# Kernel tuning notes

Measured on AMD Instinct MI355X. Metric: run time of the kernel, lower is better.

## Reference

```python
import jax, jax.numpy as jnp
import numpy as np

DIM = 512
HEAD_DIM = 32
NUM_HEADS = DIM // HEAD_DIM
SCALE = HEAD_DIM ** -0.5
SPARSE_WINDOW = 64
LN_EPS = 1e-5


def setup_inputs() -> dict:
    key = jax.random.key(0)
    ks = jax.random.split(key, 7)
    B, S = 2, 2048
    x = jax.random.normal(ks[0], (B, S, DIM), dtype=jnp.float32)
    # parameters (Linear weights stored as [in, out] for x @ W)
    W_qkv = jax.random.normal(ks[1], (DIM, 2 * DIM), dtype=jnp.float32) * (DIM ** -0.5)
    b_qkv = jnp.zeros((2 * DIM,), dtype=jnp.float32)
    W_out = jax.random.normal(ks[2], (DIM, DIM), dtype=jnp.float32) * (DIM ** -0.5)
    b_out = jnp.zeros((DIM,), dtype=jnp.float32)
    ln_gamma = jnp.ones((DIM,), dtype=jnp.float32)
    ln_beta = jnp.zeros((DIM,), dtype=jnp.float32)
    return {"x": x, "W_qkv": W_qkv, "b_qkv": b_qkv, "W_out": W_out,
            "b_out": b_out, "ln_gamma": ln_gamma, "ln_beta": ln_beta}


def _attn(x, W_qkv, b_qkv, W_out, b_out, ln_gamma, ln_beta):
    B, S, _ = x.shape
    qkv = x @ W_qkv + b_qkv                        # [B,S,2*DIM]
    qk, v = qkv[..., :DIM], qkv[..., DIM:]
    q = jax.nn.silu(qk) * SCALE                    # shared-projection nonlinear Q
    k = jnp.tanh(qk)                               # shared-projection nonlinear K
    q = q.reshape(B, S, NUM_HEADS, HEAD_DIM)
    k = k.reshape(B, S, NUM_HEADS, HEAD_DIM)
    v = v.reshape(B, S, NUM_HEADS, HEAD_DIM)
    scores = jnp.einsum('bihd,bjhd->bhij', q, k)   # [B,H,S,S]
    # sparse window: MULTIPLICATIVE zeroing outside |i-j|<=w (faithful to source)
    i = jnp.arange(S)
    band = (jnp.abs(i[:, None] - i[None, :]) <= SPARSE_WINDOW).astype(scores.dtype)
    scores = scores * band                         # zeros still enter softmax as exp(0)
    probs = jax.nn.softmax(scores, axis=-1)
    out = jnp.einsum('bhij,bjhd->bihd', probs, v).reshape(B, S, DIM)
    out = out @ W_out + b_out
    y = x + out                                    # residual (dropout is eval no-op)
    mu = jnp.mean(y, axis=-1, keepdims=True)
    var = jnp.var(y, axis=-1, keepdims=True)
    return (y - mu) * jax.lax.rsqrt(var + LN_EPS) * ln_gamma + ln_beta


def reference(x, W_qkv, b_qkv, W_out, b_out, ln_gamma, ln_beta):
    return _attn(x, W_qkv, b_qkv, W_out, b_out, ln_gamma, ln_beta)
```

## Files before the change

kernel.cpp:

```cpp
#include <hip/hip_runtime.h>
#include <cstdint>
#include <cstddef>

#define DIMX 512
#define HDIM 32
#define NHEADS 16
#define SEQ 2048
#define BATCH 2
#define MTOT (BATCH*SEQ)
#define WIN 64
#define QSCALE 0.17677669529663687f

typedef __bf16 bf16x8 __attribute__((ext_vector_type(8)));
typedef float f32x4 __attribute__((ext_vector_type(4)));

__device__ __forceinline__ unsigned short f2bf(float f){
  unsigned u = __builtin_bit_cast(unsigned, f);
  u += 0x7FFFu + ((u >> 16) & 1u);
  return (unsigned short)(u >> 16);
}
__device__ __forceinline__ float bf2f(unsigned short s){
  return __builtin_bit_cast(float, ((unsigned)s) << 16);
}
__device__ __forceinline__ unsigned pk(float a, float b){
  return (unsigned)f2bf(a) | ((unsigned)f2bf(b) << 16);
}

__device__ __forceinline__ void gl_lds16(const void* g, void* l){
  __builtin_amdgcn_global_load_lds(
      (const __attribute__((address_space(1))) unsigned*)g,
      (__attribute__((address_space(3))) unsigned*)(unsigned)(unsigned long long)l,
      16, 0, 0);
}

__global__ void k_prep(const float* __restrict__ x, unsigned short* __restrict__ xb,
                       const float* __restrict__ Wq, unsigned short* __restrict__ Wqt,
                       const float* __restrict__ Wo, unsigned short* __restrict__ Wot){
  int bx = blockIdx.x;
  if (bx < 1024){
    int i = bx * 256 + threadIdx.x;
    const float4* p = (const float4*)x + (size_t)i * 2;
    float4 a = p[0], b = p[1];
    uint4 o;
    o.x = pk(a.x, a.y); o.y = pk(a.z, a.w);
    o.z = pk(b.x, b.y); o.w = pk(b.z, b.w);
    ((uint4*)xb)[i] = o;
    return;
  }
  __shared__ float tile[32][33];
  int i = bx - 1024;
  int bxx = i % 48, byy = i / 48;
  const float* W; unsigned short* Wt; int N, n0;
  if (bxx < 32){ W = Wq; Wt = Wqt; N = 1024; n0 = bxx * 32; }
  else         { W = Wo; Wt = Wot; N = 512;  n0 = (bxx - 32) * 32; }
  int k0 = byy * 32;
  int tx = threadIdx.x & 31, ty = threadIdx.x >> 5;
  #pragma unroll
  for (int r = 0; r < 32; r += 8)
    tile[ty + r][tx] = W[(size_t)(k0 + ty + r) * N + n0 + tx];
  __syncthreads();
  #pragma unroll
  for (int r = 0; r < 32; r += 8)
    Wt[(size_t)(n0 + ty + r) * 512 + k0 + tx] = f2bf(tile[tx][ty + r]);
}

template<int MODE, int NBN>
__launch_bounds__(256)
__global__ void k_gemm(const unsigned short* __restrict__ A,
                       const unsigned short* __restrict__ Bt,
                       const float* __restrict__ bias,
                       unsigned short* __restrict__ qb,
                       unsigned short* __restrict__ kb,
                       unsigned short* __restrict__ vt,
                       float* __restrict__ vsum_p,
                       const float* __restrict__ xres,
                       float* __restrict__ y)
{
  const int K = 512;
  constexpr int NWG = 64 * NBN;
  __shared__ __align__(16) unsigned short lds[2][2][64 * 64];
  int tid = threadIdx.x;
  int wid = tid >> 6, lane = tid & 63;
  int wm = wid >> 1, wn = wid & 1;
  int lane15 = lane & 15, laneh = lane >> 4;

  int g = blockIdx.x;
  int gwi = (g & 7) * (NWG / 8) + (g >> 3);
  int bm = gwi / NBN, bn = gwi % NBN;

  f32x4 acc[2][2] = {};

  int srow_off = lane >> 3;
  int spos     = lane & 7;

  auto STAGE = [&](int buf, int kt){
    int k0 = kt * 64;
    #pragma unroll
    for (int c = 0; c < 2; ++c){
      int cidx = wid * 2 + c;
      int r = cidx * 8 + srow_off;
      int ch = spos ^ (r & 7);
      gl_lds16(A  + (size_t)(bm * 64 + r) * K + k0 + ch * 8, &lds[buf][0][cidx * 512]);
      gl_lds16(Bt + (size_t)(bn * 64 + r) * K + k0 + ch * 8, &lds[buf][1][cidx * 512]);
    }
  };

  auto COMPUTE = [&](int buf){
    #pragma unroll
    for (int kh = 0; kh < 2; ++kh){
      int chunk = kh * 4 + laneh;
      bf16x8 af[2], bf[2];
      #pragma unroll
      for (int mi = 0; mi < 2; ++mi){
        int row = wm * 32 + mi * 16 + lane15;
        af[mi] = *(const bf16x8*)&lds[buf][0][row * 64 + (chunk ^ (row & 7)) * 8];
      }
      #pragma unroll
      for (int ni = 0; ni < 2; ++ni){
        int row = wn * 32 + ni * 16 + lane15;
        bf[ni] = *(const bf16x8*)&lds[buf][1][row * 64 + (chunk ^ (row & 7)) * 8];
      }
      #pragma unroll
      for (int mi = 0; mi < 2; ++mi)
        #pragma unroll
        for (int ni = 0; ni < 2; ++ni)
          acc[mi][ni] = __builtin_amdgcn_mfma_f32_16x16x32_bf16(af[mi], bf[ni], acc[mi][ni], 0, 0, 0);
    }
  };

  STAGE(0, 0);
  __syncthreads();
  #pragma unroll
  for (int kt = 0; kt < 8; ++kt){
    if (kt < 7) STAGE((kt + 1) & 1, kt + 1);
    COMPUTE(kt & 1);
    __syncthreads();
  }

  if (MODE == 0 && bn >= 8){
    unsigned short (*tp)[72] = (unsigned short (*)[72])&lds[0][0][0];
    #pragma unroll
    for (int mi = 0; mi < 2; ++mi)
      #pragma unroll
      for (int ni = 0; ni < 2; ++ni)
        #pragma unroll
        for (int r = 0; r < 4; ++r){
          int ml = wm * 32 + mi * 16 + laneh * 4 + r;
          int nl = wn * 32 + ni * 16 + lane15;
          tp[nl][ml] = f2bf(acc[mi][ni][r] + bias[bn * 64 + nl]);
        }
    __syncthreads();
    int nl = tid >> 2, q = tid & 3;
    int h = (bn - 8) * 2 + (nl >> 5), d = nl & 31;
    int bh = (bm >> 5) * 16 + h;
    int sc = bm & 31;
    unsigned short vals[16];
    float ssum = 0.f;
    #pragma unroll
    for (int j = 0; j < 16; ++j){ vals[j] = tp[nl][q * 16 + j]; ssum += bf2f(vals[j]); }
    ssum += __shfl_xor(ssum, 1); ssum += __shfl_xor(ssum, 2);
    uint4 o0, o1;
    o0.x = (unsigned)vals[0]  | ((unsigned)vals[1]  << 16);
    o0.y = (unsigned)vals[2]  | ((unsigned)vals[3]  << 16);
    o0.z = (unsigned)vals[4]  | ((unsigned)vals[5]  << 16);
    o0.w = (unsigned)vals[6]  | ((unsigned)vals[7]  << 16);
    o1.x = (unsigned)vals[8]  | ((unsigned)vals[9]  << 16);
    o1.y = (unsigned)vals[10] | ((unsigned)vals[11] << 16);
    o1.z = (unsigned)vals[12] | ((unsigned)vals[13] << 16);
    o1.w = (unsigned)vals[14] | ((unsigned)vals[15] << 16);
    size_t vtoff = (size_t)(bh * HDIM + d) * SEQ + sc * 64 + q * 16;
    *(uint4*)(vt + vtoff) = o0;
    *(uint4*)(vt + vtoff + 8) = o1;
    if (q == 0) vsum_p[(sc * 32 + bh) * HDIM + d] = ssum;
  } else {
    #pragma unroll
    for (int mi = 0; mi < 2; ++mi){
      #pragma unroll
      for (int ni = 0; ni < 2; ++ni){
        #pragma unroll
        for (int r = 0; r < 4; ++r){
          int m = bm * 64 + wm * 32 + mi * 16 + laneh * 4 + r;
          int n = bn * 64 + wn * 32 + ni * 16 + lane15;
          float val = acc[mi][ni][r] + bias[n];
          if (MODE == 0){
            float s = val / (1.0f + __expf(-val)) * QSCALE;
            float t = tanhf(val);
            qb[(size_t)m * DIMX + n] = f2bf(s);
            kb[(size_t)m * DIMX + n] = f2bf(t);
          } else {
            size_t idx = (size_t)m * DIMX + n;
            y[idx] = val + xres[idx];
          }
        }
      }
    }
  }
}

__launch_bounds__(256)
__global__ void k_attn(const unsigned short* __restrict__ qb,
                       const unsigned short* __restrict__ kb,
                       const unsigned short* __restrict__ vt,
                       const float* __restrict__ vsum_p,
                       unsigned short* __restrict__ ao)
{
  __shared__ unsigned short p_lds[4][16][40];
  int tid = threadIdx.x, wid = tid >> 6, lane = tid & 63;
  int lane15 = lane & 15, laneh = lane >> 4;
  int bh = blockIdx.y, b = bh >> 4, h = bh & 15;
  int s0 = blockIdx.x * 64 + wid * 16;

  bf16x8 qf = *(const bf16x8*)(qb + (size_t)(b * SEQ + s0 + lane15) * DIMX + h * HDIM + laneh * 8);
  float vs0 = 0.f, vs1 = 0.f;
  #pragma unroll
  for (int c = 0; c < 32; ++c){
    vs0 += vsum_p[(c * 32 + bh) * HDIM + lane15];
    vs1 += vsum_p[(c * 32 + bh) * HDIM + 16 + lane15];
  }

  f32x4 accv[2] = {};
  float dsum[4] = {0.f, 0.f, 0.f, 0.f};

  for (int jt = 0; jt < 9; ++jt){
    int j0 = s0 - 64 + jt * 16;
    int jc = min(max(j0 + lane15, 0), SEQ - 1);
    bf16x8 kf = *(const bf16x8*)(kb + (size_t)(b * SEQ + jc) * DIMX + h * HDIM + laneh * 8);
    f32x4 z = {0.f, 0.f, 0.f, 0.f};
    f32x4 sv = __builtin_amdgcn_mfma_f32_16x16x32_bf16(qf, kf, z, 0, 0, 0);
    #pragma unroll
    for (int r = 0; r < 4; ++r){
      int i = s0 + laneh * 4 + r;
      int j = j0 + lane15;
      int dj = i - j;
      bool inb = (dj <= WIN) && (dj >= -WIN) && (j >= 0) && (j < SEQ);
      float w = inb ? (__expf(sv[r]) - 1.0f) : 0.0f;
      dsum[r] += w;
      p_lds[wid][laneh * 4 + r][(jt & 1) * 16 + lane15] = f2bf(w);
    }
    if (jt & 1){
      int jc0 = j0 - 16;
      bf16x8 pa = *(const bf16x8*)&p_lds[wid][lane15][laneh * 8];
      int jv = min(max(jc0 + laneh * 8, 0), SEQ - 8);
      bf16x8 v0 = *(const bf16x8*)(vt + (size_t)(bh * HDIM + lane15) * SEQ + jv);
      bf16x8 v1 = *(const bf16x8*)(vt + (size_t)(bh * HDIM + 16 + lane15) * SEQ + jv);
      accv[0] = __builtin_amdgcn_mfma_f32_16x16x32_bf16(pa, v0, accv[0], 0, 0, 0);
      accv[1] = __builtin_amdgcn_mfma_f32_16x16x32_bf16(pa, v1, accv[1], 0, 0, 0);
    }
  }
  {
    #pragma unroll
    for (int r = 0; r < 4; ++r)
      p_lds[wid][laneh * 4 + r][16 + lane15] = 0;
    int jc0 = s0 + 64;
    bf16x8 pa = *(const bf16x8*)&p_lds[wid][lane15][laneh * 8];
    int jv = min(max(jc0 + laneh * 8, 0), SEQ - 8);
    bf16x8 v0 = *(const bf16x8*)(vt + (size_t)(bh * HDIM + lane15) * SEQ + jv);
    bf16x8 v1 = *(const bf16x8*)(vt + (size_t)(bh * HDIM + 16 + lane15) * SEQ + jv);
    accv[0] = __builtin_amdgcn_mfma_f32_16x16x32_bf16(pa, v0, accv[0], 0, 0, 0);
    accv[1] = __builtin_amdgcn_mfma_f32_16x16x32_bf16(pa, v1, accv[1], 0, 0, 0);
  }

  #pragma unroll
  for (int r = 0; r < 4; ++r){
    float v = dsum[r];
    v += __shfl_xor(v, 1); v += __shfl_xor(v, 2);
    v += __shfl_xor(v, 4); v += __shfl_xor(v, 8);
    dsum[r] = v;
  }
  #pragma unroll
  for (int r = 0; r < 4; ++r){
    int i = s0 + laneh * 4 + r;
    float dn = (float)SEQ + dsum[r];
    float o0 = (accv[0][r] + vs0) / dn;
    float o1 = (accv[1][r] + vs1) / dn;
    size_t base = (size_t)(b * SEQ + i) * DIMX + h * HDIM;
    ao[base + lane15]      = f2bf(o0);
    ao[base + 16 + lane15] = f2bf(o1);
  }
}

__global__ void k_ln(const float* __restrict__ y, const float* __restrict__ gamma,
                     const float* __restrict__ beta, float* __restrict__ out){
  int wid = threadIdx.x >> 6, lane = threadIdx.x & 63;
  int row = blockIdx.x * 4 + wid;
  const float4* yp = (const float4*)(y + (size_t)row * DIMX);
  float4 a = yp[lane], c = yp[lane + 64];
  float s  = a.x + a.y + a.z + a.w + c.x + c.y + c.z + c.w;
  float ss = a.x*a.x + a.y*a.y + a.z*a.z + a.w*a.w + c.x*c.x + c.y*c.y + c.z*c.z + c.w*c.w;
  #pragma unroll
  for (int m = 1; m < 64; m <<= 1){ s += __shfl_xor(s, m); ss += __shfl_xor(ss, m); }
  float mu = s * (1.f / DIMX);
  float var = ss * (1.f / DIMX) - mu * mu;
  float inv = rsqrtf(var + 1e-5f);
  const float4* gp = (const float4*)gamma;
  const float4* bp = (const float4*)beta;
  float4 g0 = gp[lane], g1 = gp[lane + 64];
  float4 b0 = bp[lane], b1 = bp[lane + 64];
  float4 o0, o1;
  o0.x = (a.x - mu) * inv * g0.x + b0.x; o0.y = (a.y - mu) * inv * g0.y + b0.y;
  o0.z = (a.z - mu) * inv * g0.z + b0.z; o0.w = (a.w - mu) * inv * g0.w + b0.w;
  o1.x = (c.x - mu) * inv * g1.x + b1.x; o1.y = (c.y - mu) * inv * g1.y + b1.y;
  o1.z = (c.z - mu) * inv * g1.z + b1.z; o1.w = (c.w - mu) * inv * g1.w + b1.w;
  float4* op = (float4*)(out + (size_t)row * DIMX);
  op[lane] = o0; op[lane + 64] = o1;
}

extern "C" void kernel_launch(void* const* d_in, const int* in_sizes, int n_in,
                              void* d_out, int out_size, void* d_ws, size_t ws_size,
                              hipStream_t stream){
  const float* x      = (const float*)d_in[0];
  const float* W_qkv  = (const float*)d_in[1];
  const float* b_qkv  = (const float*)d_in[2];
  const float* W_out  = (const float*)d_in[3];
  const float* b_out  = (const float*)d_in[4];
  const float* gamma  = (const float*)d_in[5];
  const float* beta   = (const float*)d_in[6];
  float* out = (float*)d_out;

  char* ws = (char*)d_ws;
  size_t off = 0;
  auto alloc = [&](size_t bytes){ void* p = ws + off; off += (bytes + 255) & ~(size_t)255; return p; };
  unsigned short* xb  = (unsigned short*)alloc((size_t)MTOT * DIMX * 2);
  unsigned short* wqt = (unsigned short*)alloc((size_t)1024 * 512 * 2);
  unsigned short* wot = (unsigned short*)alloc((size_t)512 * 512 * 2);
  unsigned short* qb  = (unsigned short*)alloc((size_t)MTOT * DIMX * 2);
  unsigned short* kb  = (unsigned short*)alloc((size_t)MTOT * DIMX * 2);
  unsigned short* vt  = (unsigned short*)alloc((size_t)32 * HDIM * SEQ * 2);
  float*          vsm = (float*)alloc((size_t)32 * 32 * HDIM * 4);
  unsigned short* ao  = (unsigned short*)alloc((size_t)MTOT * DIMX * 2);
  float*          yb  = (float*)alloc((size_t)MTOT * DIMX * 4);

  k_prep<<<1792, 256, 0, stream>>>(x, xb, W_qkv, wqt, W_out, wot);
  k_gemm<0, 16><<<1024, 256, 0, stream>>>(xb, wqt, b_qkv, qb, kb, vt, vsm, nullptr, nullptr);
  k_attn<<<dim3(32, 32), 256, 0, stream>>>(qb, kb, vt, vsm, ao);
  k_gemm<1, 8><<<512, 256, 0, stream>>>(ao, wot, b_out, nullptr, nullptr, nullptr, nullptr, x, yb);
  k_ln  <<<MTOT / 4, 256, 0, stream>>>(yb, gamma, beta, out);
}
```

Baseline: 51.59 us.

## Enlarge QKV GEMM M-tile to 128 and store residual intermediate in bf16

The GEMM is templated on the M-tile size. The QKV projection now uses 128-row tiles in 512 workgroups, which halves the partial V-sum chunks and widens the V transpose stores to 32 elements per thread. The output projection now reads the bf16 copy of x as its residual and writes y in bf16, so the LayerNorm kernel reads half the bytes. Both changes aim to cut memory traffic and launch granularity, at the cost of fewer workgroups for the QKV GEMM and extra rounding of the residual and pre-LayerNorm values to bf16.

```diff
diff --git a/kernel.cpp b/kernel.cpp
--- a/kernel.cpp
+++ b/kernel.cpp
@@ -64,7 +64,7 @@
     Wt[(size_t)(n0 + ty + r) * 512 + k0 + tx] = f2bf(tile[tx][ty + r]);
 }
 
-template<int MODE, int NBN>
+template<int MODE, int BM, int NBM, int NBN>
 __launch_bounds__(256)
 __global__ void k_gemm(const unsigned short* __restrict__ A,
                        const unsigned short* __restrict__ Bt,
@@ -73,12 +73,14 @@
                        unsigned short* __restrict__ kb,
                        unsigned short* __restrict__ vt,
                        float* __restrict__ vsum_p,
-                       const float* __restrict__ xres,
-                       float* __restrict__ y)
+                       const unsigned short* __restrict__ xb,
+                       unsigned short* __restrict__ yb)
 {
   const int K = 512;
-  constexpr int NWG = 64 * NBN;
-  __shared__ __align__(16) unsigned short lds[2][2][64 * 64];
+  constexpr int NWG = NBM * NBN;
+  constexpr int MF  = BM / 32;
+  __shared__ __align__(16) unsigned short ldsA[2][BM * 64];
+  __shared__ __align__(16) unsigned short ldsB[2][64 * 64];
   int tid = threadIdx.x;
   int wid = tid >> 6, lane = tid & 63;
   int wm = wid >> 1, wn = wid & 1;
@@ -88,20 +90,26 @@
   int gwi = (g & 7) * (NWG / 8) + (g >> 3);
   int bm = gwi / NBN, bn = gwi % NBN;
 
-  f32x4 acc[2][2] = {};
+  f32x4 acc[MF][2] = {};
 
   int srow_off = lane >> 3;
   int spos     = lane & 7;
 
   auto STAGE = [&](int buf, int kt){
     int k0 = kt * 64;
+    #pragma unroll
+    for (int c = 0; c < MF; ++c){
+      int cidx = wid * MF + c;
+      int r = cidx * 8 + srow_off;
+      int ch = spos ^ (r & 7);
+      gl_lds16(A + (size_t)(bm * BM + r) * K + k0 + ch * 8, &ldsA[buf][cidx * 512]);
+    }
     #pragma unroll
     for (int c = 0; c < 2; ++c){
       int cidx = wid * 2 + c;
       int r = cidx * 8 + srow_off;
       int ch = spos ^ (r & 7);
-      gl_lds16(A  + (size_t)(bm * 64 + r) * K + k0 + ch * 8, &lds[buf][0][cidx * 512]);
-      gl_lds16(Bt + (size_t)(bn * 64 + r) * K + k0 + ch * 8, &lds[buf][1][cidx * 512]);
+      gl_lds16(Bt + (size_t)(bn * 64 + r) * K + k0 + ch * 8, &ldsB[buf][cidx * 512]);
     }
   };
 
@@ -109,22 +117,22 @@
     #pragma unroll
     for (int kh = 0; kh < 2; ++kh){
       int chunk = kh * 4 + laneh;
-      bf16x8 af[2], bf[2];
-      #pragma unroll
-      for (int mi = 0; mi < 2; ++mi){
-        int row = wm * 32 + mi * 16 + lane15;
-        af[mi] = *(const bf16x8*)&lds[buf][0][row * 64 + (chunk ^ (row & 7)) * 8];
+      bf16x8 af[MF], bfv[2];
+      #pragma unroll
+      for (int mi = 0; mi < MF; ++mi){
+        int row = wm * (BM / 2) + mi * 16 + lane15;
+        af[mi] = *(const bf16x8*)&ldsA[buf][row * 64 + (chunk ^ (row & 7)) * 8];
       }
       #pragma unroll
       for (int ni = 0; ni < 2; ++ni){
         int row = wn * 32 + ni * 16 + lane15;
-        bf[ni] = *(const bf16x8*)&lds[buf][1][row * 64 + (chunk ^ (row & 7)) * 8];
+        bfv[ni] = *(const bf16x8*)&ldsB[buf][row * 64 + (chunk ^ (row & 7)) * 8];
       }
       #pragma unroll
-      for (int mi = 0; mi < 2; ++mi)
+      for (int mi = 0; mi < MF; ++mi)
         #pragma unroll
         for (int ni = 0; ni < 2; ++ni)
-          acc[mi][ni] = __builtin_amdgcn_mfma_f32_16x16x32_bf16(af[mi], bf[ni], acc[mi][ni], 0, 0, 0);
+          acc[mi][ni] = __builtin_amdgcn_mfma_f32_16x16x32_bf16(af[mi], bfv[ni], acc[mi][ni], 0, 0, 0);
     }
   };
 
@@ -138,48 +146,46 @@
   }
 
   if (MODE == 0 && bn >= 8){
-    unsigned short (*tp)[72] = (unsigned short (*)[72])&lds[0][0][0];
-    #pragma unroll
-    for (int mi = 0; mi < 2; ++mi)
+    unsigned short (*tp)[136] = (unsigned short (*)[136])&ldsA[0][0];
+    #pragma unroll
+    for (int mi = 0; mi < MF; ++mi)
       #pragma unroll
       for (int ni = 0; ni < 2; ++ni)
         #pragma unroll
         for (int r = 0; r < 4; ++r){
-          int ml = wm * 32 + mi * 16 + laneh * 4 + r;
+          int ml = wm * (BM / 2) + mi * 16 + laneh * 4 + r;
           int nl = wn * 32 + ni * 16 + lane15;
           tp[nl][ml] = f2bf(acc[mi][ni][r] + bias[bn * 64 + nl]);
         }
     __syncthreads();
     int nl = tid >> 2, q = tid & 3;
     int h = (bn - 8) * 2 + (nl >> 5), d = nl & 31;
-    int bh = (bm >> 5) * 16 + h;
-    int sc = bm & 31;
-    unsigned short vals[16];
+    int b = bm >> 4, sc = bm & 15;
+    int bh = b * 16 + h;
+    uint4 v4[4];
     float ssum = 0.f;
     #pragma unroll
-    for (int j = 0; j < 16; ++j){ vals[j] = tp[nl][q * 16 + j]; ssum += bf2f(vals[j]); }
+    for (int p = 0; p < 4; ++p){
+      v4[p] = *(const uint4*)&tp[nl][q * 32 + p * 8];
+      const unsigned* w = (const unsigned*)&v4[p];
+      #pragma unroll
+      for (int j = 0; j < 4; ++j){
+        ssum += bf2f((unsigned short)(w[j] & 0xffff)) + bf2f((unsigned short)(w[j] >> 16));
+      }
+    }
     ssum += __shfl_xor(ssum, 1); ssum += __shfl_xor(ssum, 2);
-    uint4 o0, o1;
-    o0.x = (unsigned)vals[0]  | ((unsigned)vals[1]  << 16);
-    o0.y = (unsigned)vals[2]  | ((unsigned)vals[3]  << 16);
-    o0.z = (unsigned)vals[4]  | ((unsigned)vals[5]  << 16);
-    o0.w = (unsigned)vals[6]  | ((unsigned)vals[7]  << 16);
-    o1.x = (unsigned)vals[8]  | ((unsigned)vals[9]  << 16);
-    o1.y = (unsigned)vals[10] | ((unsigned)vals[11] << 16);
-    o1.z = (unsigned)vals[12] | ((unsigned)vals[13] << 16);
-    o1.w = (unsigned)vals[14] | ((unsigned)vals[15] << 16);
-    size_t vtoff = (size_t)(bh * HDIM + d) * SEQ + sc * 64 + q * 16;
-    *(uint4*)(vt + vtoff) = o0;
-    *(uint4*)(vt + vtoff + 8) = o1;
+    size_t vtoff = (size_t)(bh * HDIM + d) * SEQ + sc * 128 + q * 32;
+    #pragma unroll
+    for (int p = 0; p < 4; ++p) *(uint4*)(vt + vtoff + p * 8) = v4[p];
     if (q == 0) vsum_p[(sc * 32 + bh) * HDIM + d] = ssum;
   } else {
     #pragma unroll
-    for (int mi = 0; mi < 2; ++mi){
+    for (int mi = 0; mi < MF; ++mi){
       #pragma unroll
       for (int ni = 0; ni < 2; ++ni){
         #pragma unroll
         for (int r = 0; r < 4; ++r){
-          int m = bm * 64 + wm * 32 + mi * 16 + laneh * 4 + r;
+          int m = bm * BM + wm * (BM / 2) + mi * 16 + laneh * 4 + r;
           int n = bn * 64 + wn * 32 + ni * 16 + lane15;
           float val = acc[mi][ni][r] + bias[n];
           if (MODE == 0){
@@ -189,7 +195,7 @@
             kb[(size_t)m * DIMX + n] = f2bf(t);
           } else {
             size_t idx = (size_t)m * DIMX + n;
-            y[idx] = val + xres[idx];
+            yb[idx] = f2bf(val + bf2f(xb[idx]));
           }
         }
       }
@@ -213,7 +219,7 @@
   bf16x8 qf = *(const bf16x8*)(qb + (size_t)(b * SEQ + s0 + lane15) * DIMX + h * HDIM + laneh * 8);
   float vs0 = 0.f, vs1 = 0.f;
   #pragma unroll
-  for (int c = 0; c < 32; ++c){
+  for (int c = 0; c < 16; ++c){
     vs0 += vsum_p[(c * 32 + bh) * HDIM + lane15];
     vs1 += vsum_p[(c * 32 + bh) * HDIM + 16 + lane15];
   }
@@ -279,30 +285,37 @@
   }
 }
 
-__global__ void k_ln(const float* __restrict__ y, const float* __restrict__ gamma,
+__global__ void k_ln(const unsigned short* __restrict__ yb, const float* __restrict__ gamma,
                      const float* __restrict__ beta, float* __restrict__ out){
   int wid = threadIdx.x >> 6, lane = threadIdx.x & 63;
   int row = blockIdx.x * 4 + wid;
-  const float4* yp = (const float4*)(y + (size_t)row * DIMX);
-  float4 a = yp[lane], c = yp[lane + 64];
-  float s  = a.x + a.y + a.z + a.w + c.x + c.y + c.z + c.w;
-  float ss = a.x*a.x + a.y*a.y + a.z*a.z + a.w*a.w + c.x*c.x + c.y*c.y + c.z*c.z + c.w*c.w;
+  uint4 u = *(const uint4*)(yb + (size_t)row * DIMX + lane * 8);
+  const unsigned* w = (const unsigned*)&u;
+  float v[8];
+  #pragma unroll
+  for (int j = 0; j < 4; ++j){
+    v[2*j]   = bf2f((unsigned short)(w[j] & 0xffff));
+    v[2*j+1] = bf2f((unsigned short)(w[j] >> 16));
+  }
+  float s = 0.f, ss = 0.f;
+  #pragma unroll
+  for (int j = 0; j < 8; ++j){ s += v[j]; ss += v[j] * v[j]; }
   #pragma unroll
   for (int m = 1; m < 64; m <<= 1){ s += __shfl_xor(s, m); ss += __shfl_xor(ss, m); }
   float mu = s * (1.f / DIMX);
   float var = ss * (1.f / DIMX) - mu * mu;
   float inv = rsqrtf(var + 1e-5f);
-  const float4* gp = (const float4*)gamma;
-  const float4* bp = (const float4*)beta;
-  float4 g0 = gp[lane], g1 = gp[lane + 64];
-  float4 b0 = bp[lane], b1 = bp[lane + 64];
+  float4 g0 = *(const float4*)(gamma + lane * 8);
+  float4 g1 = *(const float4*)(gamma + lane * 8 + 4);
+  float4 b0 = *(const float4*)(beta + lane * 8);
+  float4 b1 = *(const float4*)(beta + lane * 8 + 4);
   float4 o0, o1;
-  o0.x = (a.x - mu) * inv * g0.x + b0.x; o0.y = (a.y - mu) * inv * g0.y + b0.y;
-  o0.z = (a.z - mu) * inv * g0.z + b0.z; o0.w = (a.w - mu) * inv * g0.w + b0.w;
-  o1.x = (c.x - mu) * inv * g1.x + b1.x; o1.y = (c.y - mu) * inv * g1.y + b1.y;
-  o1.z = (c.z - mu) * inv * g1.z + b1.z; o1.w = (c.w - mu) * inv * g1.w + b1.w;
-  float4* op = (float4*)(out + (size_t)row * DIMX);
-  op[lane] = o0; op[lane + 64] = o1;
+  o0.x = (v[0] - mu) * inv * g0.x + b0.x; o0.y = (v[1] - mu) * inv * g0.y + b0.y;
+  o0.z = (v[2] - mu) * inv * g0.z + b0.z; o0.w = (v[3] - mu) * inv * g0.w + b0.w;
+  o1.x = (v[4] - mu) * inv * g1.x + b1.x; o1.y = (v[5] - mu) * inv * g1.y + b1.y;
+  o1.z = (v[6] - mu) * inv * g1.z + b1.z; o1.w = (v[7] - mu) * inv * g1.w + b1.w;
+  float* op = out + (size_t)row * DIMX + lane * 8;
+  *(float4*)op = o0; *(float4*)(op + 4) = o1;
 }
 
 extern "C" void kernel_launch(void* const* d_in, const int* in_sizes, int n_in,
@@ -326,13 +339,13 @@
   unsigned short* qb  = (unsigned short*)alloc((size_t)MTOT * DIMX * 2);
   unsigned short* kb  = (unsigned short*)alloc((size_t)MTOT * DIMX * 2);
   unsigned short* vt  = (unsigned short*)alloc((size_t)32 * HDIM * SEQ * 2);
-  float*          vsm = (float*)alloc((size_t)32 * 32 * HDIM * 4);
+  float*          vsm = (float*)alloc((size_t)16 * 32 * HDIM * 4);
   unsigned short* ao  = (unsigned short*)alloc((size_t)MTOT * DIMX * 2);
-  float*          yb  = (float*)alloc((size_t)MTOT * DIMX * 4);
+  unsigned short* yb  = (unsigned short*)alloc((size_t)MTOT * DIMX * 2);
 
   k_prep<<<1792, 256, 0, stream>>>(x, xb, W_qkv, wqt, W_out, wot);
-  k_gemm<0, 16><<<1024, 256, 0, stream>>>(xb, wqt, b_qkv, qb, kb, vt, vsm, nullptr, nullptr);
+  k_gemm<0, 128, 32, 16><<<512, 256, 0, stream>>>(xb, wqt, b_qkv, qb, kb, vt, vsm, nullptr, nullptr);
   k_attn<<<dim3(32, 32), 256, 0, stream>>>(qb, kb, vt, vsm, ao);
-  k_gemm<1, 8><<<512, 256, 0, stream>>>(ao, wot, b_out, nullptr, nullptr, nullptr, nullptr, x, yb);
+  k_gemm<1, 64, 64, 8><<<512, 256, 0, stream>>>(ao, wot, b_out, nullptr, nullptr, nullptr, nullptr, xb, yb);
   k_ln  <<<MTOT / 4, 256, 0, stream>>>(yb, gamma, beta, out);
 }
```

Result: faster. 48.88 us (-5.3%).
